# Performance work log

Hardware: AMD Instinct MI355X
Metric: run time of the kernel (lower is better)

## Reference

```python
import jax, jax.numpy as jnp
import numpy as np

N_NODES = 50000
N_EDGES = 800000


def setup_inputs() -> dict:
    key = jax.random.key(0)
    ks = jax.random.split(key, 9)
    d, h, hd = 128, 4, 32
    s = 1.0 / np.sqrt(d)
    return {
        "x": jax.random.normal(ks[0], (N_NODES, d), jnp.float32),
        "edge_index": jax.random.randint(ks[1], (2, N_EDGES), 0, N_NODES, jnp.int32),
        "W0": jax.random.normal(ks[2], (d, d), jnp.float32) * s,
        "att_l0": jax.random.normal(ks[3], (h, hd), jnp.float32) * s,
        "att_r0": jax.random.normal(ks[4], (h, hd), jnp.float32) * s,
        "b0": jnp.zeros((d,), jnp.float32),
        "W1": jax.random.normal(ks[5], (d, d), jnp.float32) * s,
        "att_l1": jax.random.normal(ks[6], (h, hd), jnp.float32) * s,
        "att_r1": jax.random.normal(ks[7], (h, hd), jnp.float32) * s,
        "b1": jnp.zeros((hd,), jnp.float32),
    }


def _gat_layer(x, src, dst, W, att_l, att_r, bias, concat):
    # x: [N, F_in]; W: [H*D, F_in] (torch Linear layout); att_*: [H, D]
    n = x.shape[0]
    h, d = att_l.shape
    hx = (x @ W.T).reshape(n, h, d)                     # [N,H,D]
    al = jnp.einsum('nhd,hd->nh', hx, att_l)            # [N,H]
    ar = jnp.einsum('nhd,hd->nh', hx, att_r)
    att = al[src] + ar[dst]                             # [E,H]
    att = jax.nn.leaky_relu(att, negative_slope=0.2)
    # segment softmax over destination nodes
    m = jax.ops.segment_max(att, dst, num_segments=n)   # [N,H]
    att = jnp.exp(att - m[dst])
    ssum = jax.ops.segment_sum(att, dst, num_segments=n)
    att = att / (ssum[dst] + 1e-9)                      # [E,H]
    msgs = att[:, :, None] * hx[src]                    # [E,H,D]
    out = jax.ops.segment_sum(msgs, dst, num_segments=n)  # [N,H,D]
    if concat:
        out = out.reshape(n, h * d)
    else:
        out = out.mean(axis=1)
    return out + bias


def reference(x, edge_index, W0, att_l0, att_r0, b0, W1, att_l1, att_r1, b1):
    src, dst = edge_index[0], edge_index[1]
    x = _gat_layer(x, src, dst, W0, att_l0, att_r0, b0, concat=True)
    x = jax.nn.relu(x)  # dropout is identity in eval mode
    x = _gat_layer(x, src, dst, W1, att_l1, att_r1, b1, concat=False)
    return x
```

## Files before the change

### kernel.cpp

```cpp
#include <hip/hip_runtime.h>
#include <hip/hip_bf16.h>

#define H 4
#define D 32
#define F 128
#define MAXDEG 64
#define DEGSTRIDE 16

typedef __attribute__((ext_vector_type(8))) short bf16x8;
typedef __attribute__((ext_vector_type(4))) float f32x4;

__device__ __forceinline__ short f2bf(float v) {
    __hip_bfloat16 h = __float2bfloat16(v);
    return *reinterpret_cast<short*>(&h);
}
__device__ __forceinline__ float bf2f(short s) {
    __hip_bfloat16 h = *reinterpret_cast<__hip_bfloat16*>(&s);
    return __bfloat162float(h);
}

__device__ __forceinline__
void gemm_body(int bid, int nblocks, const float* __restrict__ X,
               const float* __restrict__ W, const float* __restrict__ attl,
               const float* __restrict__ attr, __hip_bfloat16* __restrict__ HXB,
               float* __restrict__ AL, float* __restrict__ AR, int ntiles) {
    const int wave = threadIdx.x >> 6;
    const int lane = threadIdx.x & 63;
    const int m    = lane & 15;
    const int q    = lane >> 4;
    const int q8   = q * 8;

    bf16x8 Bhi[2][4], Blo[2][4];
#pragma unroll
    for (int j = 0; j < 2; ++j) {
        const int fout = wave * 32 + j * 16 + m;
#pragma unroll
        for (int kc = 0; kc < 4; ++kc) {
            const float* wp = W + (size_t)fout * F + kc * 32 + q8;
            float4 w0 = *reinterpret_cast<const float4*>(wp);
            float4 w1 = *reinterpret_cast<const float4*>(wp + 4);
            float wv[8] = {w0.x, w0.y, w0.z, w0.w, w1.x, w1.y, w1.z, w1.w};
#pragma unroll
            for (int t = 0; t < 8; ++t) {
                short h = f2bf(wv[t]);
                Bhi[j][kc][t] = h;
                Blo[j][kc][t] = f2bf(wv[t] - bf2f(h));
            }
        }
    }
    const float alw0  = attl[wave * 32 + m];
    const float alw16 = attl[wave * 32 + 16 + m];
    const float arw0  = attr[wave * 32 + m];
    const float arw16 = attr[wave * 32 + 16 + m];

    for (int tile = bid; tile < ntiles; tile += nblocks) {
        const int node0 = tile * 16;
        bf16x8 Ahi[4], Alo[4];
        const float* xp = X + (size_t)(node0 + m) * F + q8;
#pragma unroll
        for (int kc = 0; kc < 4; ++kc) {
            float4 x0 = *reinterpret_cast<const float4*>(xp + kc * 32);
            float4 x1 = *reinterpret_cast<const float4*>(xp + kc * 32 + 4);
            float xv[8] = {x0.x, x0.y, x0.z, x0.w, x1.x, x1.y, x1.z, x1.w};
#pragma unroll
            for (int t = 0; t < 8; ++t) {
                short h = f2bf(xv[t]);
                Ahi[kc][t] = h;
                Alo[kc][t] = f2bf(xv[t] - bf2f(h));
            }
        }
        f32x4 acc0 = {0.f, 0.f, 0.f, 0.f};
        f32x4 acc1 = {0.f, 0.f, 0.f, 0.f};
#pragma unroll
        for (int kc = 0; kc < 4; ++kc) {
            acc0 = __builtin_amdgcn_mfma_f32_16x16x32_bf16(Ahi[kc], Bhi[0][kc], acc0, 0, 0, 0);
            acc1 = __builtin_amdgcn_mfma_f32_16x16x32_bf16(Ahi[kc], Bhi[1][kc], acc1, 0, 0, 0);
            acc0 = __builtin_amdgcn_mfma_f32_16x16x32_bf16(Ahi[kc], Blo[0][kc], acc0, 0, 0, 0);
            acc1 = __builtin_amdgcn_mfma_f32_16x16x32_bf16(Ahi[kc], Blo[1][kc], acc1, 0, 0, 0);
            acc0 = __builtin_amdgcn_mfma_f32_16x16x32_bf16(Alo[kc], Bhi[0][kc], acc0, 0, 0, 0);
            acc1 = __builtin_amdgcn_mfma_f32_16x16x32_bf16(Alo[kc], Bhi[1][kc], acc1, 0, 0, 0);
        }
        const int row0 = node0 + q * 4;
        const int col0 = wave * 32 + m;
#pragma unroll
        for (int r = 0; r < 4; ++r) {
            HXB[(size_t)(row0 + r) * F + col0]      = __float2bfloat16(acc0[r]);
            HXB[(size_t)(row0 + r) * F + col0 + 16] = __float2bfloat16(acc1[r]);
            float pal = acc0[r] * alw0 + acc1[r] * alw16;
            float par = acc0[r] * arw0 + acc1[r] * arw16;
#pragma unroll
            for (int o = 1; o < 16; o <<= 1) {
                pal += __shfl_xor(pal, o);
                par += __shfl_xor(par, o);
            }
            if (m == 0) {
                AL[(size_t)(row0 + r) * H + wave] = pal;
                AR[(size_t)(row0 + r) * H + wave] = par;
            }
        }
    }
}

__device__ __forceinline__
void wconv_body(const float* __restrict__ W1, __hip_bfloat16* __restrict__ W1hi,
                __hip_bfloat16* __restrict__ W1lo) {
    for (int i = threadIdx.x; i < F * F; i += 256) {
        float v = W1[i];
        short hi = f2bf(v);
        *reinterpret_cast<short*>(&W1hi[i]) = hi;
        *reinterpret_cast<short*>(&W1lo[i]) = f2bf(v - bf2f(hi));
    }
}

__device__ __forceinline__
void scatter_body(int rawBid, int base, const int* __restrict__ ei, int E,
                  int* __restrict__ deg16, unsigned short* __restrict__ ssrc2u,
                  int per) {
    const int c     = rawBid & 7;
    const int strip = (rawBid - base) >> 3;
    const int lo = c * per, hi = lo + per;
    int ebase = strip * 1024 + (int)threadIdx.x * 4;
    if (ebase >= E) return;
    if (ebase + 3 < E) {
        int4 s4 = *reinterpret_cast<const int4*>(ei + ebase);
        int4 d4 = *reinterpret_cast<const int4*>(ei + E + ebase);
        if (d4.x >= lo && d4.x < hi) {
            int s = atomicAdd(&deg16[d4.x * DEGSTRIDE], 1);
            if (s < MAXDEG) ssrc2u[d4.x * MAXDEG + s] = (unsigned short)s4.x;
        }
        if (d4.y >= lo && d4.y < hi) {
            int s = atomicAdd(&deg16[d4.y * DEGSTRIDE], 1);
            if (s < MAXDEG) ssrc2u[d4.y * MAXDEG + s] = (unsigned short)s4.y;
        }
        if (d4.z >= lo && d4.z < hi) {
            int s = atomicAdd(&deg16[d4.z * DEGSTRIDE], 1);
            if (s < MAXDEG) ssrc2u[d4.z * MAXDEG + s] = (unsigned short)s4.z;
        }
        if (d4.w >= lo && d4.w < hi) {
            int s = atomicAdd(&deg16[d4.w * DEGSTRIDE], 1);
            if (s < MAXDEG) ssrc2u[d4.w * MAXDEG + s] = (unsigned short)s4.w;
        }
    } else {
        for (int e = ebase; e < E; ++e) {
            int src = ei[e], dst = ei[E + e];
            if (dst >= lo && dst < hi) {
                int s = atomicAdd(&deg16[dst * DEGSTRIDE], 1);
                if (s < MAXDEG) ssrc2u[dst * MAXDEG + s] = (unsigned short)src;
            }
        }
    }
}

__global__ __launch_bounds__(256)
void k_pre(const float* __restrict__ X, const float* __restrict__ W0,
           const float* __restrict__ attl0, const float* __restrict__ attr0,
           __hip_bfloat16* __restrict__ HXB0, float* __restrict__ AL0,
           float* __restrict__ AR0, int ntiles, int gemm_blocks,
           const float* __restrict__ W1, __hip_bfloat16* __restrict__ W1hi,
           __hip_bfloat16* __restrict__ W1lo,
           const int* __restrict__ ei, int E,
           int* __restrict__ deg16, unsigned short* __restrict__ ssrc2u, int per) {
    const int bid = blockIdx.x;
    if (bid < gemm_blocks)
        gemm_body(bid, gemm_blocks, X, W0, attl0, attr0, HXB0, AL0, AR0, ntiles);
    else if (bid == gemm_blocks)
        wconv_body(W1, W1hi, W1lo);
    else
        scatter_body(bid, gemm_blocks + 1, ei, E, deg16, ssrc2u, per);
}

__global__ __launch_bounds__(256)
void k_aggr_gemm(const unsigned short* __restrict__ ssrc2u, const int* __restrict__ deg16,
                 const float* __restrict__ AL0, const float* __restrict__ AR0,
                 const __hip_bfloat16* __restrict__ HXB0, const float* __restrict__ b0,
                 const __hip_bfloat16* __restrict__ W1hi, const __hip_bfloat16* __restrict__ W1lo,
                 const float* __restrict__ attl1, const float* __restrict__ attr1,
                 __hip_bfloat16* __restrict__ HXB1, float* __restrict__ AL1,
                 float* __restrict__ AR1) {
    __shared__ float xs[16][132];
    __shared__ int   sidx[4][MAXDEG];
    __shared__ float sw[4][MAXDEG][H];
    const int g = threadIdx.x >> 6;
    const int t = threadIdx.x & 63;
    const int h = t >> 4;
    const int node0 = blockIdx.x * 16;

    for (int i = 0; i < 4; ++i) {
        const int n = node0 + g * 4 + i;
        const int cnt = min(deg16[n * DEGSTRIDE], MAXDEG);
        const float4 ar4 = *reinterpret_cast<const float4*>(AR0 + (size_t)n * H);
        if (t < cnt) {
            int s = ssrc2u[n * MAXDEG + t];
            sidx[g][t] = s;
            float4 al4 = *reinterpret_cast<const float4*>(AL0 + (size_t)s * H);
            float a0 = al4.x + ar4.x; a0 = a0 > 0.f ? a0 : 0.2f * a0;
            float a1 = al4.y + ar4.y; a1 = a1 > 0.f ? a1 : 0.2f * a1;
            float a2 = al4.z + ar4.z; a2 = a2 > 0.f ? a2 : 0.2f * a2;
            float a3 = al4.w + ar4.w; a3 = a3 > 0.f ? a3 : 0.2f * a3;
            sw[g][t][0] = __expf(a0);
            sw[g][t][1] = __expf(a1);
            sw[g][t][2] = __expf(a2);
            sw[g][t][3] = __expf(a3);
        }
        __builtin_amdgcn_wave_barrier();
        float accx = 0.f, accy = 0.f, wsum = 0.f;
        int e = 0;
        for (; e + 4 <= cnt; e += 4) {
            int s0 = sidx[g][e], s1 = sidx[g][e + 1], s2 = sidx[g][e + 2], s3 = sidx[g][e + 3];
            float w0 = sw[g][e][h], w1 = sw[g][e + 1][h], w2 = sw[g][e + 2][h], w3 = sw[g][e + 3][h];
            float2 f0 = __bfloat1622float2(*reinterpret_cast<const __hip_bfloat162*>(HXB0 + (size_t)s0 * F + 2 * t));
            float2 f1 = __bfloat1622float2(*reinterpret_cast<const __hip_bfloat162*>(HXB0 + (size_t)s1 * F + 2 * t));
            float2 f2 = __bfloat1622float2(*reinterpret_cast<const __hip_bfloat162*>(HXB0 + (size_t)s2 * F + 2 * t));
            float2 f3 = __bfloat1622float2(*reinterpret_cast<const __hip_bfloat162*>(HXB0 + (size_t)s3 * F + 2 * t));
            accx += w0 * f0.x + w1 * f1.x + w2 * f2.x + w3 * f3.x;
            accy += w0 * f0.y + w1 * f1.y + w2 * f2.y + w3 * f3.y;
            wsum += (w0 + w1) + (w2 + w3);
        }
        for (; e < cnt; ++e) {
            int s = sidx[g][e];
            float w = sw[g][e][h];
            float2 fv = __bfloat1622float2(*reinterpret_cast<const __hip_bfloat162*>(HXB0 + (size_t)s * F + 2 * t));
            accx += w * fv.x;
            accy += w * fv.y;
            wsum += w;
        }
        float inv = 1.f / (wsum + 1e-9f);
        const int row = g * 4 + i;
        xs[row][2 * t]     = fmaxf(accx * inv + b0[2 * t], 0.f);
        xs[row][2 * t + 1] = fmaxf(accy * inv + b0[2 * t + 1], 0.f);
        __builtin_amdgcn_wave_barrier();
    }
    __syncthreads();

    const int wave = g;
    const int m  = t & 15;
    const int q  = t >> 4;
    const int q8 = q * 8;

    bf16x8 Bhi[2][4], Blo[2][4];
#pragma unroll
    for (int j = 0; j < 2; ++j) {
        const int fout = wave * 32 + j * 16 + m;
#pragma unroll
        for (int kc = 0; kc < 4; ++kc) {
            Bhi[j][kc] = *reinterpret_cast<const bf16x8*>(W1hi + (size_t)fout * F + kc * 32 + q8);
            Blo[j][kc] = *reinterpret_cast<const bf16x8*>(W1lo + (size_t)fout * F + kc * 32 + q8);
        }
    }
    bf16x8 Ahi[4], Alo[4];
#pragma unroll
    for (int kc = 0; kc < 4; ++kc) {
        const float* xp = &xs[m][kc * 32 + q8];
        float4 x0 = *reinterpret_cast<const float4*>(xp);
        float4 x1 = *reinterpret_cast<const float4*>(xp + 4);
        float xv[8] = {x0.x, x0.y, x0.z, x0.w, x1.x, x1.y, x1.z, x1.w};
#pragma unroll
        for (int u = 0; u < 8; ++u) {
            short hi = f2bf(xv[u]);
            Ahi[kc][u] = hi;
            Alo[kc][u] = f2bf(xv[u] - bf2f(hi));
        }
    }
    f32x4 acc0 = {0.f, 0.f, 0.f, 0.f};
    f32x4 acc1 = {0.f, 0.f, 0.f, 0.f};
#pragma unroll
    for (int kc = 0; kc < 4; ++kc) {
        acc0 = __builtin_amdgcn_mfma_f32_16x16x32_bf16(Ahi[kc], Bhi[0][kc], acc0, 0, 0, 0);
        acc1 = __builtin_amdgcn_mfma_f32_16x16x32_bf16(Ahi[kc], Bhi[1][kc], acc1, 0, 0, 0);
        acc0 = __builtin_amdgcn_mfma_f32_16x16x32_bf16(Ahi[kc], Blo[0][kc], acc0, 0, 0, 0);
        acc1 = __builtin_amdgcn_mfma_f32_16x16x32_bf16(Ahi[kc], Blo[1][kc], acc1, 0, 0, 0);
        acc0 = __builtin_amdgcn_mfma_f32_16x16x32_bf16(Alo[kc], Bhi[0][kc], acc0, 0, 0, 0);
        acc1 = __builtin_amdgcn_mfma_f32_16x16x32_bf16(Alo[kc], Bhi[1][kc], acc1, 0, 0, 0);
    }
    const float alw0  = attl1[wave * 32 + m];
    const float alw16 = attl1[wave * 32 + 16 + m];
    const float arw0  = attr1[wave * 32 + m];
    const float arw16 = attr1[wave * 32 + 16 + m];
    const int row0 = node0 + q * 4;
    const int col0 = wave * 32 + m;
#pragma unroll
    for (int r = 0; r < 4; ++r) {
        HXB1[(size_t)(row0 + r) * F + col0]      = __float2bfloat16(acc0[r]);
        HXB1[(size_t)(row0 + r) * F + col0 + 16] = __float2bfloat16(acc1[r]);
        float pal = acc0[r] * alw0 + acc1[r] * alw16;
        float par = acc0[r] * arw0 + acc1[r] * arw16;
#pragma unroll
        for (int o = 1; o < 16; o <<= 1) {
            pal += __shfl_xor(pal, o);
            par += __shfl_xor(par, o);
        }
        if (m == 0) {
            AL1[(size_t)(row0 + r) * H + wave] = pal;
            AR1[(size_t)(row0 + r) * H + wave] = par;
        }
    }
}

__global__ __launch_bounds__(256)
void k_aggr1(const unsigned short* __restrict__ ssrc2u, const int* __restrict__ deg16,
             const float* __restrict__ AL, const float* __restrict__ AR,
             const __hip_bfloat16* __restrict__ HXB, const float* __restrict__ bias,
             float* __restrict__ out, int N) {
    __shared__ int   sidx[4][MAXDEG];
    __shared__ float sw[4][MAXDEG][H];
    const int g = threadIdx.x >> 6;
    const int t = threadIdx.x & 63;
    const int n = blockIdx.x * 4 + g;
    if (n >= N) return;
    const int h = t >> 4;
    const int cnt = min(deg16[n * DEGSTRIDE], MAXDEG);
    const float4 ar4 = *reinterpret_cast<const float4*>(AR + (size_t)n * H);
    if (t < cnt) {
        int s = ssrc2u[n * MAXDEG + t];
        sidx[g][t] = s;
        float4 al4 = *reinterpret_cast<const float4*>(AL + (size_t)s * H);
        float a0 = al4.x + ar4.x; a0 = a0 > 0.f ? a0 : 0.2f * a0;
        float a1 = al4.y + ar4.y; a1 = a1 > 0.f ? a1 : 0.2f * a1;
        float a2 = al4.z + ar4.z; a2 = a2 > 0.f ? a2 : 0.2f * a2;
        float a3 = al4.w + ar4.w; a3 = a3 > 0.f ? a3 : 0.2f * a3;
        sw[g][t][0] = __expf(a0);
        sw[g][t][1] = __expf(a1);
        sw[g][t][2] = __expf(a2);
        sw[g][t][3] = __expf(a3);
    }
    __builtin_amdgcn_wave_barrier();
    float accx = 0.f, accy = 0.f, wsum = 0.f;
    int e = 0;
    for (; e + 4 <= cnt; e += 4) {
        int s0 = sidx[g][e], s1 = sidx[g][e + 1], s2 = sidx[g][e + 2], s3 = sidx[g][e + 3];
        float w0 = sw[g][e][h], w1 = sw[g][e + 1][h], w2 = sw[g][e + 2][h], w3 = sw[g][e + 3][h];
        float2 f0 = __bfloat1622float2(*reinterpret_cast<const __hip_bfloat162*>(HXB + (size_t)s0 * F + 2 * t));
        float2 f1 = __bfloat1622float2(*reinterpret_cast<const __hip_bfloat162*>(HXB + (size_t)s1 * F + 2 * t));
        float2 f2 = __bfloat1622float2(*reinterpret_cast<const __hip_bfloat162*>(HXB + (size_t)s2 * F + 2 * t));
        float2 f3 = __bfloat1622float2(*reinterpret_cast<const __hip_bfloat162*>(HXB + (size_t)s3 * F + 2 * t));
        accx += w0 * f0.x + w1 * f1.x + w2 * f2.x + w3 * f3.x;
        accy += w0 * f0.y + w1 * f1.y + w2 * f2.y + w3 * f3.y;
        wsum += (w0 + w1) + (w2 + w3);
    }
    for (; e < cnt; ++e) {
        int s = sidx[g][e];
        float w = sw[g][e][h];
        float2 fv = __bfloat1622float2(*reinterpret_cast<const __hip_bfloat162*>(HXB + (size_t)s * F + 2 * t));
        accx += w * fv.x;
        accy += w * fv.y;
        wsum += w;
    }
    float inv = 1.f / (wsum + 1e-9f);
    float vx = accx * inv, vy = accy * inv;
    vx += __shfl_xor(vx, 16); vx += __shfl_xor(vx, 32);
    vy += __shfl_xor(vy, 16); vy += __shfl_xor(vy, 32);
    if (t < 16) {
        float2 o;
        o.x = 0.25f * vx + bias[2 * t];
        o.y = 0.25f * vy + bias[2 * t + 1];
        *reinterpret_cast<float2*>(out + (size_t)n * D + 2 * t) = o;
    }
}

extern "C" void kernel_launch(void* const* d_in, const int* in_sizes, int n_in,
                              void* d_out, int out_size, void* d_ws, size_t ws_size,
                              hipStream_t stream) {
    const float* x     = (const float*)d_in[0];
    const int*   ei    = (const int*)d_in[1];
    const float* W0    = (const float*)d_in[2];
    const float* attl0 = (const float*)d_in[3];
    const float* attr0 = (const float*)d_in[4];
    const float* b0    = (const float*)d_in[5];
    const float* W1    = (const float*)d_in[6];
    const float* attl1 = (const float*)d_in[7];
    const float* attr1 = (const float*)d_in[8];
    const float* b1    = (const float*)d_in[9];

    const int N = in_sizes[0] / F;
    const int E = in_sizes[1] / 2;
    const int ntiles = N / 16;
    const int per = (N + 7) / 8;

    char* p = (char*)d_ws;
    __hip_bfloat16* HXB0 = (__hip_bfloat16*)p;  p += (size_t)N * F * 2;
    __hip_bfloat16* HXB1 = (__hip_bfloat16*)p;  p += (size_t)N * F * 2;
    __hip_bfloat16* W1hi = (__hip_bfloat16*)p;  p += (size_t)F * F * 2;
    __hip_bfloat16* W1lo = (__hip_bfloat16*)p;  p += (size_t)F * F * 2;
    float* AL0 = (float*)p;                     p += (size_t)N * H * 4;
    float* AR0 = (float*)p;                     p += (size_t)N * H * 4;
    float* AL1 = (float*)p;                     p += (size_t)N * H * 4;
    float* AR1 = (float*)p;                     p += (size_t)N * H * 4;
    unsigned short* ssrc2u = (unsigned short*)p; p += (size_t)N * MAXDEG * 2;
    int* deg16 = (int*)p;

    hipMemsetAsync(deg16, 0, (size_t)N * DEGSTRIDE * sizeof(int), stream);

    const int gemm_blocks = 625;
    const int nstrips = (E + 1023) / 1024;
    const int total_blocks = gemm_blocks + 1 + 8 * nstrips;

    k_pre<<<total_blocks, 256, 0, stream>>>(x, W0, attl0, attr0, HXB0, AL0, AR0,
                                            ntiles, gemm_blocks, W1, W1hi, W1lo,
                                            ei, E, deg16, ssrc2u, per);

    k_aggr_gemm<<<ntiles, 256, 0, stream>>>(ssrc2u, deg16, AL0, AR0, HXB0, b0,
                                            W1hi, W1lo, attl1, attr1,
                                            HXB1, AL1, AR1);

    k_aggr1<<<(N + 3) / 4, 256, 0, stream>>>(ssrc2u, deg16, AL1, AR1, HXB1, b1,
                                             (float*)d_out, N);
}
```

Measured before the change: 239.0 us.

## Split CSR scatter across kernels and overlap it with first-half aggregation

The edge scatter that builds per-destination adjacency lists is split by destination range. Nodes in the first half are scattered alongside the layer-0 GEMM. Nodes in the second half are scattered in a second kernel while the first half of the fused aggregation+GEMM tiles runs, and a third kernel then handles the remaining tiles. The degree counters drop their 16-int padding, and the gather loop now issues 16 loads at a time over neighbour lists zero-padded to a multiple of 16 to get more memory-level parallelism. The cost is an extra launch, each scatter pass rereading the whole edge list, more atomic contention on the packed counters, and wasted loads for padded neighbours.

```diff
diff --git a/kernel.cpp b/kernel.cpp
--- a/kernel.cpp
+++ b/kernel.cpp
@@ -5,7 +5,7 @@
 #define D 32
 #define F 128
 #define MAXDEG 64
-#define DEGSTRIDE 16
+#define PF 16
 
 typedef __attribute__((ext_vector_type(8))) short bf16x8;
 typedef __attribute__((ext_vector_type(4))) float f32x4;
@@ -113,38 +113,33 @@
 }
 
 __device__ __forceinline__
-void scatter_body(int rawBid, int base, const int* __restrict__ ei, int E,
-                  int* __restrict__ deg16, unsigned short* __restrict__ ssrc2u,
-                  int per) {
-    const int c     = rawBid & 7;
-    const int strip = (rawBid - base) >> 3;
-    const int lo = c * per, hi = lo + per;
-    int ebase = strip * 1024 + (int)threadIdx.x * 4;
-    if (ebase >= E) return;
-    if (ebase + 3 < E) {
-        int4 s4 = *reinterpret_cast<const int4*>(ei + ebase);
-        int4 d4 = *reinterpret_cast<const int4*>(ei + E + ebase);
+void scatter_body(int sbid, const int* __restrict__ ei, int E, int lo, int hi,
+                  int* __restrict__ deg, unsigned short* __restrict__ ssrc2u) {
+    int base = (sbid * 256 + (int)threadIdx.x) * 4;
+    if (base + 3 < E) {
+        int4 s4 = *reinterpret_cast<const int4*>(ei + base);
+        int4 d4 = *reinterpret_cast<const int4*>(ei + E + base);
         if (d4.x >= lo && d4.x < hi) {
-            int s = atomicAdd(&deg16[d4.x * DEGSTRIDE], 1);
+            int s = atomicAdd(&deg[d4.x], 1);
             if (s < MAXDEG) ssrc2u[d4.x * MAXDEG + s] = (unsigned short)s4.x;
         }
         if (d4.y >= lo && d4.y < hi) {
-            int s = atomicAdd(&deg16[d4.y * DEGSTRIDE], 1);
+            int s = atomicAdd(&deg[d4.y], 1);
             if (s < MAXDEG) ssrc2u[d4.y * MAXDEG + s] = (unsigned short)s4.y;
         }
         if (d4.z >= lo && d4.z < hi) {
-            int s = atomicAdd(&deg16[d4.z * DEGSTRIDE], 1);
+            int s = atomicAdd(&deg[d4.z], 1);
             if (s < MAXDEG) ssrc2u[d4.z * MAXDEG + s] = (unsigned short)s4.z;
         }
         if (d4.w >= lo && d4.w < hi) {
-            int s = atomicAdd(&deg16[d4.w * DEGSTRIDE], 1);
+            int s = atomicAdd(&deg[d4.w], 1);
             if (s < MAXDEG) ssrc2u[d4.w * MAXDEG + s] = (unsigned short)s4.w;
         }
     } else {
-        for (int e = ebase; e < E; ++e) {
+        for (int e = base; e < E; ++e) {
             int src = ei[e], dst = ei[E + e];
             if (dst >= lo && dst < hi) {
-                int s = atomicAdd(&deg16[dst * DEGSTRIDE], 1);
+                int s = atomicAdd(&deg[dst], 1);
                 if (s < MAXDEG) ssrc2u[dst * MAXDEG + s] = (unsigned short)src;
             }
         }
@@ -152,47 +147,34 @@
 }
 
 __global__ __launch_bounds__(256)
-void k_pre(const float* __restrict__ X, const float* __restrict__ W0,
-           const float* __restrict__ attl0, const float* __restrict__ attr0,
-           __hip_bfloat16* __restrict__ HXB0, float* __restrict__ AL0,
-           float* __restrict__ AR0, int ntiles, int gemm_blocks,
-           const float* __restrict__ W1, __hip_bfloat16* __restrict__ W1hi,
-           __hip_bfloat16* __restrict__ W1lo,
-           const int* __restrict__ ei, int E,
-           int* __restrict__ deg16, unsigned short* __restrict__ ssrc2u, int per) {
+void k_A(const float* __restrict__ X, const float* __restrict__ W0,
+         const float* __restrict__ attl0, const float* __restrict__ attr0,
+         __hip_bfloat16* __restrict__ HXB0, float* __restrict__ AL0,
+         float* __restrict__ AR0, int ntiles, int gemm_blocks,
+         const float* __restrict__ W1, __hip_bfloat16* __restrict__ W1hi,
+         __hip_bfloat16* __restrict__ W1lo,
+         const int* __restrict__ ei, int E, int nsplit,
+         int* __restrict__ deg, unsigned short* __restrict__ ssrc2u) {
     const int bid = blockIdx.x;
     if (bid < gemm_blocks)
         gemm_body(bid, gemm_blocks, X, W0, attl0, attr0, HXB0, AL0, AR0, ntiles);
     else if (bid == gemm_blocks)
         wconv_body(W1, W1hi, W1lo);
     else
-        scatter_body(bid, gemm_blocks + 1, ei, E, deg16, ssrc2u, per);
-}
-
-__global__ __launch_bounds__(256)
-void k_aggr_gemm(const unsigned short* __restrict__ ssrc2u, const int* __restrict__ deg16,
-                 const float* __restrict__ AL0, const float* __restrict__ AR0,
-                 const __hip_bfloat16* __restrict__ HXB0, const float* __restrict__ b0,
-                 const __hip_bfloat16* __restrict__ W1hi, const __hip_bfloat16* __restrict__ W1lo,
-                 const float* __restrict__ attl1, const float* __restrict__ attr1,
-                 __hip_bfloat16* __restrict__ HXB1, float* __restrict__ AL1,
-                 float* __restrict__ AR1) {
-    __shared__ float xs[16][132];
-    __shared__ int   sidx[4][MAXDEG];
-    __shared__ float sw[4][MAXDEG][H];
-    const int g = threadIdx.x >> 6;
-    const int t = threadIdx.x & 63;
-    const int h = t >> 4;
-    const int node0 = blockIdx.x * 16;
-
-    for (int i = 0; i < 4; ++i) {
-        const int n = node0 + g * 4 + i;
-        const int cnt = min(deg16[n * DEGSTRIDE], MAXDEG);
-        const float4 ar4 = *reinterpret_cast<const float4*>(AR0 + (size_t)n * H);
+        scatter_body(bid - gemm_blocks - 1, ei, E, 0, nsplit, deg, ssrc2u);
+}
+
+__device__ __forceinline__
+int stage_node(int g, int t, int n, const unsigned short* __restrict__ ssrc2u,
+               const int* __restrict__ deg, const float* __restrict__ AL,
+               const float4 ar4, int (*sidx)[MAXDEG], float (*sw)[MAXDEG][H]) {
+    const int cnt  = min(deg[n], MAXDEG);
+    const int rcnt = (cnt + PF - 1) & ~(PF - 1);
+    if (t < rcnt) {
         if (t < cnt) {
             int s = ssrc2u[n * MAXDEG + t];
             sidx[g][t] = s;
-            float4 al4 = *reinterpret_cast<const float4*>(AL0 + (size_t)s * H);
+            float4 al4 = *reinterpret_cast<const float4*>(AL + (size_t)s * H);
             float a0 = al4.x + ar4.x; a0 = a0 > 0.f ? a0 : 0.2f * a0;
             float a1 = al4.y + ar4.y; a1 = a1 > 0.f ? a1 : 0.2f * a1;
             float a2 = al4.z + ar4.z; a2 = a2 > 0.f ? a2 : 0.2f * a2;
@@ -201,29 +183,60 @@
             sw[g][t][1] = __expf(a1);
             sw[g][t][2] = __expf(a2);
             sw[g][t][3] = __expf(a3);
-        }
-        __builtin_amdgcn_wave_barrier();
+        } else {
+            sidx[g][t] = 0;
+            sw[g][t][0] = 0.f; sw[g][t][1] = 0.f; sw[g][t][2] = 0.f; sw[g][t][3] = 0.f;
+        }
+    }
+    __builtin_amdgcn_wave_barrier();
+    return rcnt;
+}
+
+__device__ __forceinline__
+void gather_node(int g, int t, int h, int rcnt, const __hip_bfloat16* __restrict__ HXB,
+                 const int (*sidx)[MAXDEG], const float (*sw)[MAXDEG][H],
+                 float& accx, float& accy, float& wsum) {
+    for (int base = 0; base < rcnt; base += PF) {
+        __hip_bfloat162 v[PF];
+#pragma unroll
+        for (int j = 0; j < PF; ++j) {
+            int s = sidx[g][base + j];
+            v[j] = *reinterpret_cast<const __hip_bfloat162*>(HXB + (size_t)s * F + 2 * t);
+        }
+#pragma unroll
+        for (int j = 0; j < PF; ++j) {
+            float w = sw[g][base + j][h];
+            float2 f = __bfloat1622float2(v[j]);
+            accx += w * f.x;
+            accy += w * f.y;
+            wsum += w;
+        }
+    }
+}
+
+__device__ __forceinline__
+void aggr_gemm_body(int tile, const unsigned short* __restrict__ ssrc2u,
+                    const int* __restrict__ deg,
+                    const float* __restrict__ AL0, const float* __restrict__ AR0,
+                    const __hip_bfloat16* __restrict__ HXB0, const float* __restrict__ b0,
+                    const __hip_bfloat16* __restrict__ W1hi, const __hip_bfloat16* __restrict__ W1lo,
+                    const float* __restrict__ attl1, const float* __restrict__ attr1,
+                    __hip_bfloat16* __restrict__ HXB1, float* __restrict__ AL1,
+                    float* __restrict__ AR1) {
+    __shared__ float xs[16][132];
+    __shared__ int   sidx[4][MAXDEG];
+    __shared__ float sw[4][MAXDEG][H];
+    const int g = threadIdx.x >> 6;
+    const int t = threadIdx.x & 63;
+    const int h = t >> 4;
+    const int node0 = tile * 16;
+
+    for (int i = 0; i < 4; ++i) {
+        const int n = node0 + g * 4 + i;
+        const float4 ar4 = *reinterpret_cast<const float4*>(AR0 + (size_t)n * H);
+        int rcnt = stage_node(g, t, n, ssrc2u, deg, AL0, ar4, sidx, sw);
         float accx = 0.f, accy = 0.f, wsum = 0.f;
-        int e = 0;
-        for (; e + 4 <= cnt; e += 4) {
-            int s0 = sidx[g][e], s1 = sidx[g][e + 1], s2 = sidx[g][e + 2], s3 = sidx[g][e + 3];
-            float w0 = sw[g][e][h], w1 = sw[g][e + 1][h], w2 = sw[g][e + 2][h], w3 = sw[g][e + 3][h];
-            float2 f0 = __bfloat1622float2(*reinterpret_cast<const __hip_bfloat162*>(HXB0 + (size_t)s0 * F + 2 * t));
-            float2 f1 = __bfloat1622float2(*reinterpret_cast<const __hip_bfloat162*>(HXB0 + (size_t)s1 * F + 2 * t));
-            float2 f2 = __bfloat1622float2(*reinterpret_cast<const __hip_bfloat162*>(HXB0 + (size_t)s2 * F + 2 * t));
-            float2 f3 = __bfloat1622float2(*reinterpret_cast<const __hip_bfloat162*>(HXB0 + (size_t)s3 * F + 2 * t));
-            accx += w0 * f0.x + w1 * f1.x + w2 * f2.x + w3 * f3.x;
-            accy += w0 * f0.y + w1 * f1.y + w2 * f2.y + w3 * f3.y;
-            wsum += (w0 + w1) + (w2 + w3);
-        }
-        for (; e < cnt; ++e) {
-            int s = sidx[g][e];
-            float w = sw[g][e][h];
-            float2 fv = __bfloat1622float2(*reinterpret_cast<const __hip_bfloat162*>(HXB0 + (size_t)s * F + 2 * t));
-            accx += w * fv.x;
-            accy += w * fv.y;
-            wsum += w;
-        }
+        gather_node(g, t, h, rcnt, HXB0, sidx, sw, accx, accy, wsum);
         float inv = 1.f / (wsum + 1e-9f);
         const int row = g * 4 + i;
         xs[row][2 * t]     = fmaxf(accx * inv + b0[2 * t], 0.f);
@@ -297,10 +310,39 @@
 }
 
 __global__ __launch_bounds__(256)
-void k_aggr1(const unsigned short* __restrict__ ssrc2u, const int* __restrict__ deg16,
-             const float* __restrict__ AL, const float* __restrict__ AR,
-             const __hip_bfloat16* __restrict__ HXB, const float* __restrict__ bias,
-             float* __restrict__ out, int N) {
+void k_B(const int* __restrict__ ei, int E, int nsplit, int scatter_blocks,
+         int* __restrict__ deg, unsigned short* __restrict__ ssrc2u,
+         const float* __restrict__ AL0, const float* __restrict__ AR0,
+         const __hip_bfloat16* __restrict__ HXB0, const float* __restrict__ b0,
+         const __hip_bfloat16* __restrict__ W1hi, const __hip_bfloat16* __restrict__ W1lo,
+         const float* __restrict__ attl1, const float* __restrict__ attr1,
+         __hip_bfloat16* __restrict__ HXB1, float* __restrict__ AL1,
+         float* __restrict__ AR1, int N) {
+    const int bid = blockIdx.x;
+    if (bid < scatter_blocks)
+        scatter_body(bid, ei, E, nsplit, N, deg, ssrc2u);
+    else
+        aggr_gemm_body(bid - scatter_blocks, ssrc2u, deg, AL0, AR0, HXB0, b0,
+                       W1hi, W1lo, attl1, attr1, HXB1, AL1, AR1);
+}
+
+__global__ __launch_bounds__(256)
+void k_C(int tile0, const unsigned short* __restrict__ ssrc2u, const int* __restrict__ deg,
+         const float* __restrict__ AL0, const float* __restrict__ AR0,
+         const __hip_bfloat16* __restrict__ HXB0, const float* __restrict__ b0,
+         const __hip_bfloat16* __restrict__ W1hi, const __hip_bfloat16* __restrict__ W1lo,
+         const float* __restrict__ attl1, const float* __restrict__ attr1,
+         __hip_bfloat16* __restrict__ HXB1, float* __restrict__ AL1,
+         float* __restrict__ AR1) {
+    aggr_gemm_body(tile0 + blockIdx.x, ssrc2u, deg, AL0, AR0, HXB0, b0,
+                   W1hi, W1lo, attl1, attr1, HXB1, AL1, AR1);
+}
+
+__global__ __launch_bounds__(256)
+void k_D(const unsigned short* __restrict__ ssrc2u, const int* __restrict__ deg,
+         const float* __restrict__ AL, const float* __restrict__ AR,
+         const __hip_bfloat16* __restrict__ HXB, const float* __restrict__ bias,
+         float* __restrict__ out, int N) {
     __shared__ int   sidx[4][MAXDEG];
     __shared__ float sw[4][MAXDEG][H];
     const int g = threadIdx.x >> 6;
@@ -308,43 +350,10 @@
     const int n = blockIdx.x * 4 + g;
     if (n >= N) return;
     const int h = t >> 4;
-    const int cnt = min(deg16[n * DEGSTRIDE], MAXDEG);
     const float4 ar4 = *reinterpret_cast<const float4*>(AR + (size_t)n * H);
-    if (t < cnt) {
-        int s = ssrc2u[n * MAXDEG + t];
-        sidx[g][t] = s;
-        float4 al4 = *reinterpret_cast<const float4*>(AL + (size_t)s * H);
-        float a0 = al4.x + ar4.x; a0 = a0 > 0.f ? a0 : 0.2f * a0;
-        float a1 = al4.y + ar4.y; a1 = a1 > 0.f ? a1 : 0.2f * a1;
-        float a2 = al4.z + ar4.z; a2 = a2 > 0.f ? a2 : 0.2f * a2;
-        float a3 = al4.w + ar4.w; a3 = a3 > 0.f ? a3 : 0.2f * a3;
-        sw[g][t][0] = __expf(a0);
-        sw[g][t][1] = __expf(a1);
-        sw[g][t][2] = __expf(a2);
-        sw[g][t][3] = __expf(a3);
-    }
-    __builtin_amdgcn_wave_barrier();
+    int rcnt = stage_node(g, t, n, ssrc2u, deg, AL, ar4, sidx, sw);
     float accx = 0.f, accy = 0.f, wsum = 0.f;
-    int e = 0;
-    for (; e + 4 <= cnt; e += 4) {
-        int s0 = sidx[g][e], s1 = sidx[g][e + 1], s2 = sidx[g][e + 2], s3 = sidx[g][e + 3];
-        float w0 = sw[g][e][h], w1 = sw[g][e + 1][h], w2 = sw[g][e + 2][h], w3 = sw[g][e + 3][h];
-        float2 f0 = __bfloat1622float2(*reinterpret_cast<const __hip_bfloat162*>(HXB + (size_t)s0 * F + 2 * t));
-        float2 f1 = __bfloat1622float2(*reinterpret_cast<const __hip_bfloat162*>(HXB + (size_t)s1 * F + 2 * t));
-        float2 f2 = __bfloat1622float2(*reinterpret_cast<const __hip_bfloat162*>(HXB + (size_t)s2 * F + 2 * t));
-        float2 f3 = __bfloat1622float2(*reinterpret_cast<const __hip_bfloat162*>(HXB + (size_t)s3 * F + 2 * t));
-        accx += w0 * f0.x + w1 * f1.x + w2 * f2.x + w3 * f3.x;
-        accy += w0 * f0.y + w1 * f1.y + w2 * f2.y + w3 * f3.y;
-        wsum += (w0 + w1) + (w2 + w3);
-    }
-    for (; e < cnt; ++e) {
-        int s = sidx[g][e];
-        float w = sw[g][e][h];
-        float2 fv = __bfloat1622float2(*reinterpret_cast<const __hip_bfloat162*>(HXB + (size_t)s * F + 2 * t));
-        accx += w * fv.x;
-        accy += w * fv.y;
-        wsum += w;
-    }
+    gather_node(g, t, h, rcnt, HXB, sidx, sw, accx, accy, wsum);
     float inv = 1.f / (wsum + 1e-9f);
     float vx = accx * inv, vy = accy * inv;
     vx += __shfl_xor(vx, 16); vx += __shfl_xor(vx, 32);
@@ -374,7 +383,8 @@
     const int N = in_sizes[0] / F;
     const int E = in_sizes[1] / 2;
     const int ntiles = N / 16;
-    const int per = (N + 7) / 8;
+    const int tsplit = ntiles / 2;
+    const int nsplit = tsplit * 16;
 
     char* p = (char*)d_ws;
     __hip_bfloat16* HXB0 = (__hip_bfloat16*)p;  p += (size_t)N * F * 2;
@@ -386,22 +396,25 @@
     float* AL1 = (float*)p;                     p += (size_t)N * H * 4;
     float* AR1 = (float*)p;                     p += (size_t)N * H * 4;
     unsigned short* ssrc2u = (unsigned short*)p; p += (size_t)N * MAXDEG * 2;
-    int* deg16 = (int*)p;
-
-    hipMemsetAsync(deg16, 0, (size_t)N * DEGSTRIDE * sizeof(int), stream);
-
-    const int gemm_blocks = 625;
-    const int nstrips = (E + 1023) / 1024;
-    const int total_blocks = gemm_blocks + 1 + 8 * nstrips;
-
-    k_pre<<<total_blocks, 256, 0, stream>>>(x, W0, attl0, attr0, HXB0, AL0, AR0,
-                                            ntiles, gemm_blocks, W1, W1hi, W1lo,
-                                            ei, E, deg16, ssrc2u, per);
-
-    k_aggr_gemm<<<ntiles, 256, 0, stream>>>(ssrc2u, deg16, AL0, AR0, HXB0, b0,
-                                            W1hi, W1lo, attl1, attr1,
-                                            HXB1, AL1, AR1);
-
-    k_aggr1<<<(N + 3) / 4, 256, 0, stream>>>(ssrc2u, deg16, AL1, AR1, HXB1, b1,
-                                             (float*)d_out, N);
-}
+    int* deg = (int*)p;
+
+    hipMemsetAsync(deg, 0, (size_t)N * sizeof(int), stream);
+
+    const int gemm_blocks    = 625;
+    const int scatter_blocks = (E / 4 + 255) / 256;
+
+    k_A<<<gemm_blocks + 1 + scatter_blocks, 256, 0, stream>>>(
+        x, W0, attl0, attr0, HXB0, AL0, AR0, ntiles, gemm_blocks,
+        W1, W1hi, W1lo, ei, E, nsplit, deg, ssrc2u);
+
+    k_B<<<scatter_blocks + tsplit, 256, 0, stream>>>(
+        ei, E, nsplit, scatter_blocks, deg, ssrc2u,
+        AL0, AR0, HXB0, b0, W1hi, W1lo, attl1, attr1, HXB1, AL1, AR1, N);
+
+    k_C<<<ntiles - tsplit, 256, 0, stream>>>(
+        tsplit, ssrc2u, deg, AL0, AR0, HXB0, b0, W1hi, W1lo,
+        attl1, attr1, HXB1, AL1, AR1);
+
+    k_D<<<(N + 3) / 4, 256, 0, stream>>>(ssrc2u, deg, AL1, AR1, HXB1, b1,
+                                         (float*)d_out, N);
+}
```

After: 237.2 us. Within noise of the previous version (-0.7%).
